# Optimization experiments

Measured on AMD Instinct MI355X. Metric: run time of the kernel, lower is better.

## Reference

```python
import jax, jax.numpy as jnp
import numpy as np

N = 256        # number of objects
HID = 768      # hidden_dim


def setup_inputs() -> dict:
    key = jax.random.key(0)
    ks = jax.random.split(key, 4)
    s1 = 1.0 / np.sqrt(2 * HID)
    s2 = 1.0 / np.sqrt(HID)
    s3 = 1.0 / np.sqrt(HID // 2)
    return {
        "object_features": jax.random.normal(ks[0], (N, HID), dtype=jnp.float32),
        "W1": jax.random.normal(ks[1], (2 * HID, HID), dtype=jnp.float32) * s1,
        "b1": jnp.zeros((HID,), dtype=jnp.float32),
        "W2": jax.random.normal(ks[2], (HID, HID // 2), dtype=jnp.float32) * s2,
        "b2": jnp.zeros((HID // 2,), dtype=jnp.float32),
        "W3": jax.random.normal(ks[3], (HID // 2, 128), dtype=jnp.float32) * s3,
        "b3": jnp.zeros((128,), dtype=jnp.float32),
    }


def reference(object_features, W1, b1, W2, b2, W3, b3):
    # All unordered pairs i < j, in the same (i, j) lexicographic order as the
    # original double loop: numpy triu_indices is row-major over i then j.
    i_idx, j_idx = np.triu_indices(N, k=1)          # each [num_pairs]
    pairs = jnp.concatenate(
        [object_features[i_idx], object_features[j_idx]], axis=-1
    )                                                # [num_pairs, 2*HID]
    h = jax.nn.relu(pairs @ W1 + b1)                 # [num_pairs, HID]
    h = jax.nn.relu(h @ W2 + b2)                     # [num_pairs, HID//2]
    return h @ W3 + b3                               # [num_pairs, 128]
```

## Files before the change

### kernel.cpp

```cpp
#include <hip/hip_runtime.h>
#include <hip/hip_bf16.h>
#include <stdint.h>

#define HID 768

typedef short bf16x8 __attribute__((ext_vector_type(8)));
typedef unsigned short ushort8_t __attribute__((ext_vector_type(8)));
typedef float f32x4 __attribute__((ext_vector_type(4)));

__device__ __forceinline__ unsigned int pack2bf(float x, float y) {
    __hip_bfloat162 h = __float22bfloat162_rn(make_float2(x, y));
    return *reinterpret_cast<unsigned int*>(&h);
}
__device__ __forceinline__ unsigned short f2bf1(float x) {
    __hip_bfloat16 h = __float2bfloat16(x);
    return *reinterpret_cast<unsigned short*>(&h);
}

__device__ __forceinline__ void gload_lds16(const void* g, void* l) {
    __builtin_amdgcn_global_load_lds(
        (const __attribute__((address_space(1))) unsigned int*)g,
        (__attribute__((address_space(3))) unsigned int*)l, 16, 0, 0);
}

__launch_bounds__(256, 2)
__global__ void prep_ab_k(const float* __restrict__ F,
                          const float* __restrict__ W1,
                          const float* __restrict__ b1,
                          const float* __restrict__ W2,
                          const float* __restrict__ W3,
                          unsigned short* __restrict__ W2t,
                          unsigned short* __restrict__ W3t,
                          float* __restrict__ AB) {
    __shared__ alignas(1024) char smem[51200];
    int b = blockIdx.x;

    if (b >= 96) {
        float (*t)[33] = (float(*)[33])smem;
        int b2 = b - 96;
        const float* in; unsigned short* op; int R, C, bx, by;
        if (b2 < 288) { in = W2; op = W2t; R = 768; C = 384; bx = b2 % 12; by = b2 / 12; }
        else          { int b3i = b2 - 288; in = W3; op = W3t; R = 384; C = 128; bx = b3i % 4; by = b3i / 4; }
        int c0 = bx * 32, r0 = by * 32;
        int tx = threadIdx.x & 31, ty = threadIdx.x >> 5;
        #pragma unroll
        for (int k = 0; k < 4; ++k)
            t[ty + 8*k][tx] = in[(size_t)(r0 + ty + 8*k) * C + c0 + tx];
        __syncthreads();
        #pragma unroll
        for (int k = 0; k < 4; ++k)
            op[(size_t)(c0 + ty + 8*k) * R + r0 + tx] = f2bf1(t[tx][ty + 8*k]);
        return;
    }

    unsigned short* fl = (unsigned short*)smem;
    float*          wt = (float*)(smem + 18432);

    int tid = threadIdx.x;
    int lane = tid & 63, wid = tid >> 6;
    int bx = b % 24, by = b / 24;
    int n0 = bx * 64, m0 = by * 64;
    const float* Wsrc = W1 + (n0 < 768 ? 0 : (size_t)768*768);
    int cb = (n0 < 768) ? n0 : n0 - 768;

    f32x4 acc[4] = {};
    float4 rf[2][2];

    #pragma unroll
    for (int s = 0; s < 4; ++s) {
        int chunk = wid*4 + s;
        int rk = chunk*4 + (lane>>4);
        int c16 = (lane&15)*4;
        gload_lds16(Wsrc + (size_t)rk*HID + cb + c16, (char*)wt + chunk*1024);
    }
    #pragma unroll
    for (int s = 0; s < 2; ++s) {
        int idx = tid + s*256;
        int r = idx >> 3, c8 = idx & 7;
        const float4* src = (const float4*)(F + (size_t)(m0 + r)*HID + c8*8);
        rf[s][0] = src[0]; rf[s][1] = src[1];
    }
    #pragma unroll
    for (int s = 0; s < 2; ++s) {
        int idx = tid + s*256;
        int r = idx >> 3, c8 = idx & 7;
        unsigned int us32[4] = { pack2bf(rf[s][0].x, rf[s][0].y), pack2bf(rf[s][0].z, rf[s][0].w),
                                 pack2bf(rf[s][1].x, rf[s][1].y), pack2bf(rf[s][1].z, rf[s][1].w) };
        *(ushort8_t*)(fl + r*72 + c8*8) = *(ushort8_t*)us32;
    }
    __syncthreads();

    for (int t = 0; t < 12; ++t) {
        int cur = t & 1;
        unsigned short* flc = fl + cur*(64*72);
        float* wtc = wt + cur*(64*64);
        if (t < 11) {
            int kk = (t+1) * 64;
            float* wtn = wt + (cur^1)*(64*64);
            #pragma unroll
            for (int s = 0; s < 4; ++s) {
                int chunk = wid*4 + s;
                int rk = chunk*4 + (lane>>4);
                int c16 = (lane&15)*4;
                gload_lds16(Wsrc + (size_t)(kk + rk)*HID + cb + c16, (char*)wtn + chunk*1024);
            }
            #pragma unroll
            for (int s = 0; s < 2; ++s) {
                int idx = tid + s*256;
                int r = idx >> 3, c8 = idx & 7;
                const float4* src = (const float4*)(F + (size_t)(m0 + r)*HID + kk + c8*8);
                rf[s][0] = src[0]; rf[s][1] = src[1];
            }
        }
        __builtin_amdgcn_s_setprio(1);
        #pragma unroll
        for (int ks = 0; ks < 2; ++ks) {
            bf16x8 a[4], bfrag;
            #pragma unroll
            for (int fm = 0; fm < 4; ++fm)
                a[fm] = *(const bf16x8*)(flc + (fm*16 + (lane&15))*72 + ks*32 + (lane>>4)*8);
            {
                int nl = wid*16 + (lane&15);
                int k0 = ks*32 + (lane>>4)*8;
                float v[8];
                #pragma unroll
                for (int d = 0; d < 8; ++d)
                    v[d] = wtc[(k0 + d)*64 + nl];
                unsigned int us[4] = { pack2bf(v[0],v[1]), pack2bf(v[2],v[3]),
                                       pack2bf(v[4],v[5]), pack2bf(v[6],v[7]) };
                bfrag = *(bf16x8*)us;
            }
            #pragma unroll
            for (int fm = 0; fm < 4; ++fm)
                acc[fm] = __builtin_amdgcn_mfma_f32_16x16x32_bf16(a[fm], bfrag, acc[fm], 0,0,0);
        }
        __builtin_amdgcn_s_setprio(0);
        if (t < 11) {
            unsigned short* fln = fl + (cur^1)*(64*72);
            #pragma unroll
            for (int s = 0; s < 2; ++s) {
                int idx = tid + s*256;
                int r = idx >> 3, c8 = idx & 7;
                unsigned int us32[4] = { pack2bf(rf[s][0].x, rf[s][0].y), pack2bf(rf[s][0].z, rf[s][0].w),
                                         pack2bf(rf[s][1].x, rf[s][1].y), pack2bf(rf[s][1].z, rf[s][1].w) };
                *(ushort8_t*)(fln + r*72 + c8*8) = *(ushort8_t*)us32;
            }
        }
        __syncthreads();
    }
    #pragma unroll
    for (int fm = 0; fm < 4; ++fm)
        #pragma unroll
        for (int q = 0; q < 4; ++q) {
            int row = m0 + fm*16 + (lane>>4)*4 + q;
            int col = n0 + wid*16 + (lane&15);
            float bias = (col < 768) ? b1[col] : 0.0f;
            AB[(size_t)row*1536 + col] = acc[fm][q] + bias;
        }
}

__launch_bounds__(1024, 1)
__global__ void fused_k(const float* __restrict__ AB,
                        const unsigned short* __restrict__ W2t,
                        const float* __restrict__ b2,
                        const unsigned short* __restrict__ W3t,
                        const float* __restrict__ b3,
                        float* __restrict__ out) {
    __shared__ alignas(1024) char smem[135168];
    unsigned short* h1b = (unsigned short*)(smem);
    unsigned short* w2b = (unsigned short*)(smem + 36864);
    unsigned short* h2  = (unsigned short*)(smem);
    unsigned short* w3b = (unsigned short*)(smem + 100352);

    int tid = threadIdx.x;
    int lane = tid & 63, wid = tid >> 6;
    int wr = wid >> 3, wc = wid & 7;
    int p0 = blockIdx.x * 128;

    int hr = tid >> 3;
    int hc = (tid & 7) * 8;
    int p = p0 + hr;
    float sdisc = sqrtf((float)(511*511 - 8*p));
    int i_me = (int)((511.0f - sdisc) * 0.5f);
    if (i_me < 0) i_me = 0; if (i_me > 254) i_me = 254;
    while (i_me < 255 && (i_me+1)*255 - (i_me+1)*i_me/2 <= p) ++i_me;
    while (i_me > 0 && i_me*255 - i_me*(i_me-1)/2 > p) --i_me;
    int j_me = i_me + 1 + (p - (i_me*255 - i_me*(i_me-1)/2));

    float4 ra[2], rb[2];

    {
        const float4* pa = (const float4*)(AB + (size_t)i_me*1536 + hc);
        const float4* pb = (const float4*)(AB + (size_t)j_me*1536 + 768 + hc);
        ra[0] = pa[0]; ra[1] = pa[1]; rb[0] = pb[0]; rb[1] = pb[1];
        unsigned int us32[4];
        #pragma unroll
        for (int u = 0; u < 2; ++u) {
            us32[u*2+0] = pack2bf(fmaxf(ra[u].x + rb[u].x, 0.f), fmaxf(ra[u].y + rb[u].y, 0.f));
            us32[u*2+1] = pack2bf(fmaxf(ra[u].z + rb[u].z, 0.f), fmaxf(ra[u].w + rb[u].w, 0.f));
        }
        *(ushort8_t*)(h1b + hr*72 + hc) = *(ushort8_t*)us32;
    }
    #pragma unroll
    for (int s = 0; s < 3; ++s) {
        int chunk = wid*3 + s;
        int row = chunk*8 + (lane>>3);
        int cg = (lane&7) ^ (row&7);
        gload_lds16(W2t + (size_t)row*HID + cg*8, (char*)w2b + chunk*1024);
    }
    __syncthreads();

    f32x4 acc2[4][3] = {};
    for (int t = 0; t < 12; ++t) {
        int cur = t & 1;
        unsigned short* h1c = h1b + cur * (128*72);
        unsigned short* w2c = w2b + cur * (384*64);
        if (t < 11) {
            int kk = (t+1) * 64;
            unsigned short* w2n = w2b + (cur^1) * (384*64);
            #pragma unroll
            for (int s = 0; s < 3; ++s) {
                int chunk = wid*3 + s;
                int row = chunk*8 + (lane>>3);
                int cg = (lane&7) ^ (row&7);
                gload_lds16(W2t + (size_t)row*HID + kk + cg*8, (char*)w2n + chunk*1024);
            }
            const float4* pa = (const float4*)(AB + (size_t)i_me*1536 + kk + hc);
            const float4* pb = (const float4*)(AB + (size_t)j_me*1536 + 768 + kk + hc);
            ra[0] = pa[0]; ra[1] = pa[1]; rb[0] = pb[0]; rb[1] = pb[1];
        }
        __builtin_amdgcn_s_setprio(1);
        #pragma unroll
        for (int ks = 0; ks < 2; ++ks) {
            bf16x8 a[4], bfr[3];
            #pragma unroll
            for (int fm = 0; fm < 4; ++fm)
                a[fm] = *(const bf16x8*)(h1c + (wr*64 + fm*16 + (lane&15))*72 + ks*32 + (lane>>4)*8);
            #pragma unroll
            for (int fn = 0; fn < 3; ++fn) {
                int n = wc*48 + fn*16 + (lane&15);
                int g = ks*4 + (lane>>4);
                bfr[fn] = *(const bf16x8*)(w2c + n*64 + ((g ^ (n&7)) * 8));
            }
            #pragma unroll
            for (int fm = 0; fm < 4; ++fm)
                #pragma unroll
                for (int fn = 0; fn < 3; ++fn)
                    acc2[fm][fn] = __builtin_amdgcn_mfma_f32_16x16x32_bf16(a[fm], bfr[fn], acc2[fm][fn], 0,0,0);
        }
        __builtin_amdgcn_s_setprio(0);
        if (t < 11) {
            unsigned short* h1n = h1b + (cur^1) * (128*72);
            unsigned int us32[4];
            #pragma unroll
            for (int u = 0; u < 2; ++u) {
                us32[u*2+0] = pack2bf(fmaxf(ra[u].x + rb[u].x, 0.f), fmaxf(ra[u].y + rb[u].y, 0.f));
                us32[u*2+1] = pack2bf(fmaxf(ra[u].z + rb[u].z, 0.f), fmaxf(ra[u].w + rb[u].w, 0.f));
            }
            *(ushort8_t*)(h1n + hr*72 + hc) = *(ushort8_t*)us32;
        }
        __syncthreads();
    }

    #pragma unroll
    for (int fn = 0; fn < 3; ++fn) {
        int col = wc*48 + fn*16 + (lane&15);
        float bb = b2[col];
        #pragma unroll
        for (int fm = 0; fm < 4; ++fm)
            #pragma unroll
            for (int q = 0; q < 4; ++q) {
                int row = wr*64 + fm*16 + (lane>>4)*4 + q;
                h2[row*392 + col] = f2bf1(fmaxf(acc2[fm][fn][q] + bb, 0.f));
            }
    }
    {
        int chunk = wid;
        int row = chunk*8 + (lane>>3);
        int cg = (lane&7) ^ (row&7);
        gload_lds16(W3t + (size_t)row*384 + cg*8, (char*)w3b + chunk*1024);
    }
    __syncthreads();

    int wrB = wid >> 2, wcB = wid & 3;
    f32x4 acc3[2][2] = {};
    for (int kt = 0; kt < 6; ++kt) {
        int cur = kt & 1;
        unsigned short* w3c = w3b + cur * (128*64);
        if (kt < 5) {
            unsigned short* w3n = w3b + (cur^1) * (128*64);
            int chunk = wid;
            int row = chunk*8 + (lane>>3);
            int cg = (lane&7) ^ (row&7);
            gload_lds16(W3t + (size_t)row*384 + (kt+1)*64 + cg*8, (char*)w3n + chunk*1024);
        }
        __builtin_amdgcn_s_setprio(1);
        #pragma unroll
        for (int ks = 0; ks < 2; ++ks) {
            bf16x8 a[2], bfr[2];
            #pragma unroll
            for (int fm = 0; fm < 2; ++fm)
                a[fm] = *(const bf16x8*)(h2 + (wrB*32 + fm*16 + (lane&15))*392 + kt*64 + ks*32 + (lane>>4)*8);
            #pragma unroll
            for (int fn = 0; fn < 2; ++fn) {
                int n = wcB*32 + fn*16 + (lane&15);
                int g = ks*4 + (lane>>4);
                bfr[fn] = *(const bf16x8*)(w3c + n*64 + ((g ^ (n&7)) * 8));
            }
            #pragma unroll
            for (int fm = 0; fm < 2; ++fm)
                #pragma unroll
                for (int fn = 0; fn < 2; ++fn)
                    acc3[fm][fn] = __builtin_amdgcn_mfma_f32_16x16x32_bf16(a[fm], bfr[fn], acc3[fm][fn], 0,0,0);
        }
        __builtin_amdgcn_s_setprio(0);
        __syncthreads();
    }
    #pragma unroll
    for (int fm = 0; fm < 2; ++fm)
        #pragma unroll
        for (int fn = 0; fn < 2; ++fn) {
            int col = wcB*32 + fn*16 + (lane&15);
            float bb = b3[col];
            #pragma unroll
            for (int q = 0; q < 4; ++q) {
                int row = p0 + wrB*32 + fm*16 + (lane>>4)*4 + q;
                out[(size_t)row*128 + col] = acc3[fm][fn][q] + bb;
            }
        }
}

extern "C" void kernel_launch(void* const* d_in, const int* in_sizes, int n_in,
                              void* d_out, int out_size, void* d_ws, size_t ws_size,
                              hipStream_t stream) {
    const float* feat = (const float*)d_in[0];
    const float* W1   = (const float*)d_in[1];
    const float* b1   = (const float*)d_in[2];
    const float* W2   = (const float*)d_in[3];
    const float* b2   = (const float*)d_in[4];
    const float* W3   = (const float*)d_in[5];
    const float* b3   = (const float*)d_in[6];
    float* out = (float*)d_out;

    char* ws = (char*)d_ws;
    unsigned short* W2t = (unsigned short*)(ws + 0);
    unsigned short* W3t = (unsigned short*)(ws + 589824);
    float*          AB  = (float*)        (ws + 688128);

    prep_ab_k<<<432, 256, 0, stream>>>(feat, W1, b1, W2, W3, W2t, W3t, AB);
    fused_k<<<255, 1024, 0, stream>>>(AB, W2t, b2, W3t, b3, out);
}
```

Before: 48.47 us.

## Halve fused kernel block to 512 threads with larger per-wave tiles

```diff
diff --git a/kernel.cpp b/kernel.cpp
--- a/kernel.cpp
+++ b/kernel.cpp
@@ -159,7 +159,7 @@
         }
 }
 
-__launch_bounds__(1024, 1)
+__launch_bounds__(512, 2)
 __global__ void fused_k(const float* __restrict__ AB,
                         const unsigned short* __restrict__ W2t,
                         const float* __restrict__ b2,
@@ -174,11 +174,11 @@
 
     int tid = threadIdx.x;
     int lane = tid & 63, wid = tid >> 6;
-    int wr = wid >> 3, wc = wid & 7;
+    int wc = wid;
     int p0 = blockIdx.x * 128;
 
-    int hr = tid >> 3;
-    int hc = (tid & 7) * 8;
+    int hr = tid >> 2;
+    int hc = (tid & 3) * 16;
     int p = p0 + hr;
     float sdisc = sqrtf((float)(511*511 - 8*p));
     int i_me = (int)((511.0f - sdisc) * 0.5f);
@@ -187,30 +187,32 @@
     while (i_me > 0 && i_me*255 - i_me*(i_me-1)/2 > p) --i_me;
     int j_me = i_me + 1 + (p - (i_me*255 - i_me*(i_me-1)/2));
 
-    float4 ra[2], rb[2];
+    float4 ra[4], rb[4];
 
     {
         const float4* pa = (const float4*)(AB + (size_t)i_me*1536 + hc);
         const float4* pb = (const float4*)(AB + (size_t)j_me*1536 + 768 + hc);
-        ra[0] = pa[0]; ra[1] = pa[1]; rb[0] = pb[0]; rb[1] = pb[1];
-        unsigned int us32[4];
-        #pragma unroll
-        for (int u = 0; u < 2; ++u) {
+        #pragma unroll
+        for (int u = 0; u < 4; ++u) { ra[u] = pa[u]; rb[u] = pb[u]; }
+        unsigned int us32[8];
+        #pragma unroll
+        for (int u = 0; u < 4; ++u) {
             us32[u*2+0] = pack2bf(fmaxf(ra[u].x + rb[u].x, 0.f), fmaxf(ra[u].y + rb[u].y, 0.f));
             us32[u*2+1] = pack2bf(fmaxf(ra[u].z + rb[u].z, 0.f), fmaxf(ra[u].w + rb[u].w, 0.f));
         }
-        *(ushort8_t*)(h1b + hr*72 + hc) = *(ushort8_t*)us32;
-    }
-    #pragma unroll
-    for (int s = 0; s < 3; ++s) {
-        int chunk = wid*3 + s;
+        *(ushort8_t*)(h1b + hr*72 + hc)     = *(ushort8_t*)(us32);
+        *(ushort8_t*)(h1b + hr*72 + hc + 8) = *(ushort8_t*)(us32 + 4);
+    }
+    #pragma unroll
+    for (int s = 0; s < 6; ++s) {
+        int chunk = wid*6 + s;
         int row = chunk*8 + (lane>>3);
         int cg = (lane&7) ^ (row&7);
         gload_lds16(W2t + (size_t)row*HID + cg*8, (char*)w2b + chunk*1024);
     }
     __syncthreads();
 
-    f32x4 acc2[4][3] = {};
+    f32x4 acc2[8][3] = {};
     for (int t = 0; t < 12; ++t) {
         int cur = t & 1;
         unsigned short* h1c = h1b + cur * (128*72);
@@ -219,23 +221,21 @@
             int kk = (t+1) * 64;
             unsigned short* w2n = w2b + (cur^1) * (384*64);
             #pragma unroll
-            for (int s = 0; s < 3; ++s) {
-                int chunk = wid*3 + s;
+            for (int s = 0; s < 6; ++s) {
+                int chunk = wid*6 + s;
                 int row = chunk*8 + (lane>>3);
                 int cg = (lane&7) ^ (row&7);
                 gload_lds16(W2t + (size_t)row*HID + kk + cg*8, (char*)w2n + chunk*1024);
             }
             const float4* pa = (const float4*)(AB + (size_t)i_me*1536 + kk + hc);
             const float4* pb = (const float4*)(AB + (size_t)j_me*1536 + 768 + kk + hc);
-            ra[0] = pa[0]; ra[1] = pa[1]; rb[0] = pb[0]; rb[1] = pb[1];
+            #pragma unroll
+            for (int u = 0; u < 4; ++u) { ra[u] = pa[u]; rb[u] = pb[u]; }
         }
         __builtin_amdgcn_s_setprio(1);
         #pragma unroll
         for (int ks = 0; ks < 2; ++ks) {
-            bf16x8 a[4], bfr[3];
-            #pragma unroll
-            for (int fm = 0; fm < 4; ++fm)
-                a[fm] = *(const bf16x8*)(h1c + (wr*64 + fm*16 + (lane&15))*72 + ks*32 + (lane>>4)*8);
+            bf16x8 bfr[3];
             #pragma unroll
             for (int fn = 0; fn < 3; ++fn) {
                 int n = wc*48 + fn*16 + (lane&15);
@@ -243,21 +243,24 @@
                 bfr[fn] = *(const bf16x8*)(w2c + n*64 + ((g ^ (n&7)) * 8));
             }
             #pragma unroll
-            for (int fm = 0; fm < 4; ++fm)
+            for (int fm = 0; fm < 8; ++fm) {
+                bf16x8 a = *(const bf16x8*)(h1c + (fm*16 + (lane&15))*72 + ks*32 + (lane>>4)*8);
                 #pragma unroll
                 for (int fn = 0; fn < 3; ++fn)
-                    acc2[fm][fn] = __builtin_amdgcn_mfma_f32_16x16x32_bf16(a[fm], bfr[fn], acc2[fm][fn], 0,0,0);
+                    acc2[fm][fn] = __builtin_amdgcn_mfma_f32_16x16x32_bf16(a, bfr[fn], acc2[fm][fn], 0,0,0);
+            }
         }
         __builtin_amdgcn_s_setprio(0);
         if (t < 11) {
             unsigned short* h1n = h1b + (cur^1) * (128*72);
-            unsigned int us32[4];
-            #pragma unroll
-            for (int u = 0; u < 2; ++u) {
+            unsigned int us32[8];
+            #pragma unroll
+            for (int u = 0; u < 4; ++u) {
                 us32[u*2+0] = pack2bf(fmaxf(ra[u].x + rb[u].x, 0.f), fmaxf(ra[u].y + rb[u].y, 0.f));
                 us32[u*2+1] = pack2bf(fmaxf(ra[u].z + rb[u].z, 0.f), fmaxf(ra[u].w + rb[u].w, 0.f));
             }
-            *(ushort8_t*)(h1n + hr*72 + hc) = *(ushort8_t*)us32;
+            *(ushort8_t*)(h1n + hr*72 + hc)     = *(ushort8_t*)(us32);
+            *(ushort8_t*)(h1n + hr*72 + hc + 8) = *(ushort8_t*)(us32 + 4);
         }
         __syncthreads();
     }
@@ -267,15 +270,16 @@
         int col = wc*48 + fn*16 + (lane&15);
         float bb = b2[col];
         #pragma unroll
-        for (int fm = 0; fm < 4; ++fm)
+        for (int fm = 0; fm < 8; ++fm)
             #pragma unroll
             for (int q = 0; q < 4; ++q) {
-                int row = wr*64 + fm*16 + (lane>>4)*4 + q;
+                int row = fm*16 + (lane>>4)*4 + q;
                 h2[row*392 + col] = f2bf1(fmaxf(acc2[fm][fn][q] + bb, 0.f));
             }
     }
-    {
-        int chunk = wid;
+    #pragma unroll
+    for (int s = 0; s < 2; ++s) {
+        int chunk = wid*2 + s;
         int row = chunk*8 + (lane>>3);
         int cg = (lane&7) ^ (row&7);
         gload_lds16(W3t + (size_t)row*384 + cg*8, (char*)w3b + chunk*1024);
@@ -283,24 +287,24 @@
     __syncthreads();
 
     int wrB = wid >> 2, wcB = wid & 3;
-    f32x4 acc3[2][2] = {};
+    f32x4 acc3[4][2] = {};
     for (int kt = 0; kt < 6; ++kt) {
         int cur = kt & 1;
         unsigned short* w3c = w3b + cur * (128*64);
         if (kt < 5) {
             unsigned short* w3n = w3b + (cur^1) * (128*64);
-            int chunk = wid;
-            int row = chunk*8 + (lane>>3);
-            int cg = (lane&7) ^ (row&7);
-            gload_lds16(W3t + (size_t)row*384 + (kt+1)*64 + cg*8, (char*)w3n + chunk*1024);
+            #pragma unroll
+            for (int s = 0; s < 2; ++s) {
+                int chunk = wid*2 + s;
+                int row = chunk*8 + (lane>>3);
+                int cg = (lane&7) ^ (row&7);
+                gload_lds16(W3t + (size_t)row*384 + (kt+1)*64 + cg*8, (char*)w3n + chunk*1024);
+            }
         }
         __builtin_amdgcn_s_setprio(1);
         #pragma unroll
         for (int ks = 0; ks < 2; ++ks) {
-            bf16x8 a[2], bfr[2];
-            #pragma unroll
-            for (int fm = 0; fm < 2; ++fm)
-                a[fm] = *(const bf16x8*)(h2 + (wrB*32 + fm*16 + (lane&15))*392 + kt*64 + ks*32 + (lane>>4)*8);
+            bf16x8 bfr[2];
             #pragma unroll
             for (int fn = 0; fn < 2; ++fn) {
                 int n = wcB*32 + fn*16 + (lane&15);
@@ -308,23 +312,25 @@
                 bfr[fn] = *(const bf16x8*)(w3c + n*64 + ((g ^ (n&7)) * 8));
             }
             #pragma unroll
-            for (int fm = 0; fm < 2; ++fm)
+            for (int fm = 0; fm < 4; ++fm) {
+                bf16x8 a = *(const bf16x8*)(h2 + (wrB*64 + fm*16 + (lane&15))*392 + kt*64 + ks*32 + (lane>>4)*8);
                 #pragma unroll
                 for (int fn = 0; fn < 2; ++fn)
-                    acc3[fm][fn] = __builtin_amdgcn_mfma_f32_16x16x32_bf16(a[fm], bfr[fn], acc3[fm][fn], 0,0,0);
+                    acc3[fm][fn] = __builtin_amdgcn_mfma_f32_16x16x32_bf16(a, bfr[fn], acc3[fm][fn], 0,0,0);
+            }
         }
         __builtin_amdgcn_s_setprio(0);
         __syncthreads();
     }
     #pragma unroll
-    for (int fm = 0; fm < 2; ++fm)
+    for (int fm = 0; fm < 4; ++fm)
         #pragma unroll
         for (int fn = 0; fn < 2; ++fn) {
             int col = wcB*32 + fn*16 + (lane&15);
             float bb = b3[col];
             #pragma unroll
             for (int q = 0; q < 4; ++q) {
-                int row = p0 + wrB*32 + fm*16 + (lane>>4)*4 + q;
+                int row = p0 + wrB*64 + fm*16 + (lane>>4)*4 + q;
                 out[(size_t)row*128 + col] = acc3[fm][fn][q] + bb;
             }
         }
@@ -348,5 +354,5 @@
     float*          AB  = (float*)        (ws + 688128);
 
     prep_ab_k<<<432, 256, 0, stream>>>(feat, W1, b1, W2, W3, W2t, W3t, AB);
-    fused_k<<<255, 1024, 0, stream>>>(AB, W2t, b2, W3t, b3, out);
-}
+    fused_k<<<255, 512, 0, stream>>>(AB, W2t, b2, W3t, b3, out);
+}
```

Result: slower. 54.09 us (+11.6%).
